# Kernel tuning notes

Hardware: AMD Instinct MI355X
Metric: run time of the kernel (lower is better)

The kernel has to match this reference:

```python
import jax, jax.numpy as jnp
import numpy as np

HEAD_DIM = 32
KS = 3        # kernel_size
DIL = 2       # dilation
SCALE = HEAD_DIM ** -0.5


def _unfold_1d(x, ks, dil):
    """Emulate nn.Unfold(ks, dil, dil*(ks-1)//2, 1) applied to x[:, :, :, None].

    x: [B, d, N]. The input is treated as an N x 1 image, so of the ks*ks
    window slots only the center width-column gathers real values; the rest
    are zero padding (faithful to the torch module).
    Returns [B, d, ks*ks, N].
    """
    B, d, N = x.shape
    pad = dil * (ks - 1) // 2
    xp = jnp.pad(x, ((0, 0), (0, 0), (pad, pad)))
    # shifted rows along the sequence (height) axis: [B, d, ks, N]
    rows = jnp.stack([xp[:, :, i * dil:i * dil + N] for i in range(ks)], axis=2)
    c = (ks - 1) // 2
    full = jnp.zeros((B, d, ks, ks, N), x.dtype).at[:, :, :, c, :].set(rows)
    return full.reshape(B, d, ks * ks, N)


def setup_inputs() -> dict:
    key = jax.random.key(0)
    kq, kk, kv = jax.random.split(key, 3)
    B, d, N = 4, 256, 8192
    return {
        "q": jax.random.normal(kq, (B, d, N), dtype=jnp.float32),
        "k": jax.random.normal(kk, (B, d, N), dtype=jnp.float32),
        "v": jax.random.normal(kv, (B, d, N), dtype=jnp.float32),
    }


def reference(q, k, v):
    B, d, N = q.shape
    h = d // HEAD_DIM
    K = KS * KS
    qh = q.reshape(B, h, HEAD_DIM, N)                       # [B,h,hd,N]
    kw = _unfold_1d(k, KS, DIL).reshape(B, h, HEAD_DIM, K, N)
    vw = _unfold_1d(v, KS, DIL).reshape(B, h, HEAD_DIM, K, N)
    attn = jnp.einsum('bhdn,bhdkn->bhnk', qh, kw) * SCALE    # [B,h,N,K]
    attn = jax.nn.softmax(attn, axis=-1)
    x = jnp.einsum('bhnk,bhdkn->bhnd', attn, vw)             # [B,h,N,hd]
    return x.transpose(0, 2, 1, 3).reshape(B, N, d)
```

## Files before the change

kernel.cpp:

```cpp
#include <hip/hip_runtime.h>


constexpr int Bn = 4;
constexpr int Dd = 256;
constexpr int Nn = 8192;
constexpr int HD = 32;
constexpr int Hh = Dd / HD;
constexpr float SCALE = 0.17677669529663687f;

typedef float vfloat4 __attribute__((ext_vector_type(4)));

__global__ __launch_bounds__(256) void dilate_attn_kernel(
    const float* __restrict__ q,
    const float* __restrict__ k,
    const float* __restrict__ v,
    float* __restrict__ out)
{
    const int tid     = threadIdx.x;
    const int lane    = tid & 63;
    const int sub     = lane & 15;
    const int quarter = lane >> 4;
    const int w       = tid >> 6;

    const int blk = blockIdx.x;
    const int bh  = blk >> 5;
    const int h   = bh & (Hh - 1);
    const int b   = bh >> 3;
    const int n0  = ((blk & 31) << 8) + (w << 6) + (sub << 2);

    const int cb = (b * Dd + h * HD + quarter * 8) * Nn + n0;
    const float* qb = q + cb;
    const float* kb = k + cb;
    const float* vb = v + cb;

    const bool hasL = (n0 >= 4);
    const bool hasR = (n0 + 4 < Nn);

    float s0[4] = {0.f, 0.f, 0.f, 0.f};
    float s1[4] = {0.f, 0.f, 0.f, 0.f};
    float s2[4] = {0.f, 0.f, 0.f, 0.f};
    #pragma unroll
    for (int c = 0; c < 8; ++c) {
        const int o = c * Nn;
        const float4 qc = *reinterpret_cast<const float4*>(qb + o);
        const float4 kc = *reinterpret_cast<const float4*>(kb + o);
        float2 km = make_float2(0.f, 0.f), kp = make_float2(0.f, 0.f);
        if (hasL) km = *reinterpret_cast<const float2*>(kb + o - 2);
        if (hasR) kp = *reinterpret_cast<const float2*>(kb + o + 4);
        s0[0] = fmaf(qc.x, km.x, s0[0]);
        s1[0] = fmaf(qc.x, kc.x, s1[0]);
        s2[0] = fmaf(qc.x, kc.z, s2[0]);
        s0[1] = fmaf(qc.y, km.y, s0[1]);
        s1[1] = fmaf(qc.y, kc.y, s1[1]);
        s2[1] = fmaf(qc.y, kc.w, s2[1]);
        s0[2] = fmaf(qc.z, kc.x, s0[2]);
        s1[2] = fmaf(qc.z, kc.z, s1[2]);
        s2[2] = fmaf(qc.z, kp.x, s2[2]);
        s0[3] = fmaf(qc.w, kc.y, s0[3]);
        s1[3] = fmaf(qc.w, kc.w, s1[3]);
        s2[3] = fmaf(qc.w, kp.y, s2[3]);
    }

    float p0[4], p1[4], p2[4];
    #pragma unroll
    for (int j = 0; j < 4; ++j) {
        float a = s0[j], bb = s1[j], cc = s2[j];
        a  += __shfl_xor(a, 16, 64);  a  += __shfl_xor(a, 32, 64);
        bb += __shfl_xor(bb, 16, 64); bb += __shfl_xor(bb, 32, 64);
        cc += __shfl_xor(cc, 16, 64); cc += __shfl_xor(cc, 32, 64);
        a *= SCALE; bb *= SCALE; cc *= SCALE;
        const float m  = fmaxf(fmaxf(a, bb), fmaxf(cc, 0.f));
        const float e0 = __expf(a - m);
        const float e1 = __expf(bb - m);
        const float e2 = __expf(cc - m);
        const float inv = 1.f / (e0 + e1 + e2 + 6.f * __expf(-m));
        p0[j] = e0 * inv; p1[j] = e1 * inv; p2[j] = e2 * inv;
    }

    float t[4][8];
    #pragma unroll
    for (int c = 0; c < 8; ++c) {
        const int o = c * Nn;
        const float4 vc = *reinterpret_cast<const float4*>(vb + o);
        float2 vm = make_float2(0.f, 0.f), vp = make_float2(0.f, 0.f);
        if (hasL) vm = *reinterpret_cast<const float2*>(vb + o - 2);
        if (hasR) vp = *reinterpret_cast<const float2*>(vb + o + 4);
        t[0][c] = fmaf(p0[0], vm.x, fmaf(p1[0], vc.x, p2[0] * vc.z));
        t[1][c] = fmaf(p0[1], vm.y, fmaf(p1[1], vc.y, p2[1] * vc.w));
        t[2][c] = fmaf(p0[2], vc.x, fmaf(p1[2], vc.z, p2[2] * vp.x));
        t[3][c] = fmaf(p0[3], vc.y, fmaf(p1[3], vc.w, p2[3] * vp.y));
    }

    float* ob = out + (b * Nn + n0) * Dd + h * HD + quarter * 8;
    #pragma unroll
    for (int j = 0; j < 4; ++j) {
        vfloat4* p = reinterpret_cast<vfloat4*>(ob + j * Dd);
        vfloat4 a = {t[j][0], t[j][1], t[j][2], t[j][3]};
        vfloat4 bq = {t[j][4], t[j][5], t[j][6], t[j][7]};
        __builtin_nontemporal_store(a, p);
        __builtin_nontemporal_store(bq, p + 1);
    }
}

extern "C" void kernel_launch(void* const* d_in, const int* in_sizes, int n_in,
                              void* d_out, int out_size, void* d_ws, size_t ws_size,
                              hipStream_t stream)
{
    const float* q = (const float*)d_in[0];
    const float* k = (const float*)d_in[1];
    const float* v = (const float*)d_in[2];
    float* out = (float*)d_out;

    const int total_threads = Bn * Hh * (Nn / 4) * 4;
    dilate_attn_kernel<<<total_threads / 256, 256, 0, stream>>>(q, k, v, out);
}
```

Before: 29.31 us.

## Stage K and V tiles with halos into LDS via direct global-to-LDS loads

K and V tiles of 32 rows by 128 columns, plus small halo columns, are copied into shared memory with global_load_lds. Neighbour taps then read from LDS instead of issuing overlapping misaligned float2 global loads. Q loads are hoisted ahead of the barrier so they overlap with the LDS fill. Blocks shrink to 128 threads, and the 36 KB of shared memory per block may limit occupancy.

```diff
diff --git a/kernel.cpp b/kernel.cpp
--- a/kernel.cpp
+++ b/kernel.cpp
@@ -1,4 +1,5 @@
 #include <hip/hip_runtime.h>
+#include <stdint.h>
 
 
 constexpr int Bn = 4;
@@ -6,34 +7,77 @@
 constexpr int Nn = 8192;
 constexpr int HD = 32;
 constexpr int Hh = Dd / HD;
+constexpr int NT = 128;
+constexpr int THREADS = 128;
 constexpr float SCALE = 0.17677669529663687f;
 
 typedef float vfloat4 __attribute__((ext_vector_type(4)));
 
-__global__ __launch_bounds__(256) void dilate_attn_kernel(
+__device__ __forceinline__ void gload_lds16(const float* g, float* l) {
+    __builtin_amdgcn_global_load_lds(
+        (const __attribute__((address_space(1))) void*)g,
+        (__attribute__((address_space(3))) void*)l, 16, 0, 0);
+}
+
+__global__ __launch_bounds__(THREADS) void dilate_attn_kernel(
     const float* __restrict__ q,
     const float* __restrict__ k,
     const float* __restrict__ v,
     float* __restrict__ out)
 {
+    __shared__ float kt[32 * NT];
+    __shared__ float vt[32 * NT];
+    __shared__ float khalo[32 * 8];
+    __shared__ float vhalo[32 * 8];
+
     const int tid     = threadIdx.x;
+    const int w       = tid >> 6;
     const int lane    = tid & 63;
-    const int sub     = lane & 15;
     const int quarter = lane >> 4;
-    const int w       = tid >> 6;
+    const int sub     = w * 16 + (lane & 15);
 
-    const int blk = blockIdx.x;
-    const int bh  = blk >> 5;
-    const int h   = bh & (Hh - 1);
-    const int b   = bh >> 3;
-    const int n0  = ((blk & 31) << 8) + (w << 6) + (sub << 2);
+    const int blk   = blockIdx.x;
+    const int bh    = blk >> 6;
+    const int blkn  = blk & 63;
+    const int h     = bh & (Hh - 1);
+    const int b     = bh >> 3;
+    const int nstart  = blkn * NT;
+    const int base_bh = (b * Dd + h * HD) * Nn;
 
-    const int cb = (b * Dd + h * HD + quarter * 8) * Nn + n0;
-    const float* qb = q + cb;
-    const float* kb = k + cb;
-    const float* vb = v + cb;
+    {
+        const int l31   = lane & 31;
+        const int rhalf = lane >> 5;
+        #pragma unroll
+        for (int i8 = 0; i8 < 8; ++i8) {
+            const int i   = w * 8 + i8;
+            const int row = 2 * i + rhalf;
+            gload_lds16(k + base_bh + row * Nn + nstart + l31 * 4, &kt[i * 256]);
+        }
+        #pragma unroll
+        for (int i8 = 0; i8 < 8; ++i8) {
+            const int i   = w * 8 + i8;
+            const int row = 2 * i + rhalf;
+            gload_lds16(v + base_bh + row * Nn + nstart + l31 * 4, &vt[i * 256]);
+        }
+        const int hch  = lane >> 1;
+        const int half = lane & 1;
+        int gcol = nstart + (half ? NT : -4);
+        gcol = gcol < 0 ? 0 : (gcol > Nn - 4 ? Nn - 4 : gcol);
+        if (w == 0) gload_lds16(k + base_bh + hch * Nn + gcol, &khalo[0]);
+        else        gload_lds16(v + base_bh + hch * Nn + gcol, &vhalo[0]);
+    }
 
-    const bool hasL = (n0 >= 4);
+    const int n0l = sub * 4;
+    const int n0  = nstart + n0l;
+    float4 qc[8];
+    const float* qb = q + base_bh + (quarter * 8) * Nn + nstart + n0l;
+    #pragma unroll
+    for (int c = 0; c < 8; ++c)
+        qc[c] = *reinterpret_cast<const float4*>(qb + c * Nn);
+
+    __syncthreads();
+
+    const bool hasL = (n0 >= 2);
     const bool hasR = (n0 + 4 < Nn);
 
     float s0[4] = {0.f, 0.f, 0.f, 0.f};
@@ -41,24 +85,26 @@
     float s2[4] = {0.f, 0.f, 0.f, 0.f};
     #pragma unroll
     for (int c = 0; c < 8; ++c) {
-        const int o = c * Nn;
-        const float4 qc = *reinterpret_cast<const float4*>(qb + o);
-        const float4 kc = *reinterpret_cast<const float4*>(kb + o);
-        float2 km = make_float2(0.f, 0.f), kp = make_float2(0.f, 0.f);
-        if (hasL) km = *reinterpret_cast<const float2*>(kb + o - 2);
-        if (hasR) kp = *reinterpret_cast<const float2*>(kb + o + 4);
-        s0[0] = fmaf(qc.x, km.x, s0[0]);
-        s1[0] = fmaf(qc.x, kc.x, s1[0]);
-        s2[0] = fmaf(qc.x, kc.z, s2[0]);
-        s0[1] = fmaf(qc.y, km.y, s0[1]);
-        s1[1] = fmaf(qc.y, kc.y, s1[1]);
-        s2[1] = fmaf(qc.y, kc.w, s2[1]);
-        s0[2] = fmaf(qc.z, kc.x, s0[2]);
-        s1[2] = fmaf(qc.z, kc.z, s1[2]);
-        s2[2] = fmaf(qc.z, kp.x, s2[2]);
-        s0[3] = fmaf(qc.w, kc.y, s0[3]);
-        s1[3] = fmaf(qc.w, kc.w, s1[3]);
-        s2[3] = fmaf(qc.w, kp.y, s2[3]);
+        const int row = quarter * 8 + c;
+        const float4 kc = *reinterpret_cast<const float4*>(&kt[row * NT + n0l]);
+        const float* pm = (sub == 0)  ? &khalo[row * 8 + 2] : &kt[row * NT + n0l - 2];
+        const float* pp = (sub == 31) ? &khalo[row * 8 + 4] : &kt[row * NT + n0l + 4];
+        const float2 kmr = *reinterpret_cast<const float2*>(pm);
+        const float2 kpr = *reinterpret_cast<const float2*>(pp);
+        const float2 km = hasL ? kmr : make_float2(0.f, 0.f);
+        const float2 kp = hasR ? kpr : make_float2(0.f, 0.f);
+        s0[0] = fmaf(qc[c].x, km.x, s0[0]);
+        s1[0] = fmaf(qc[c].x, kc.x, s1[0]);
+        s2[0] = fmaf(qc[c].x, kc.z, s2[0]);
+        s0[1] = fmaf(qc[c].y, km.y, s0[1]);
+        s1[1] = fmaf(qc[c].y, kc.y, s1[1]);
+        s2[1] = fmaf(qc[c].y, kc.w, s2[1]);
+        s0[2] = fmaf(qc[c].z, kc.x, s0[2]);
+        s1[2] = fmaf(qc[c].z, kc.z, s1[2]);
+        s2[2] = fmaf(qc[c].z, kp.x, s2[2]);
+        s0[3] = fmaf(qc[c].w, kc.y, s0[3]);
+        s1[3] = fmaf(qc[c].w, kc.w, s1[3]);
+        s2[3] = fmaf(qc[c].w, kp.y, s2[3]);
     }
 
     float p0[4], p1[4], p2[4];
@@ -80,11 +126,14 @@
     float t[4][8];
     #pragma unroll
     for (int c = 0; c < 8; ++c) {
-        const int o = c * Nn;
-        const float4 vc = *reinterpret_cast<const float4*>(vb + o);
-        float2 vm = make_float2(0.f, 0.f), vp = make_float2(0.f, 0.f);
-        if (hasL) vm = *reinterpret_cast<const float2*>(vb + o - 2);
-        if (hasR) vp = *reinterpret_cast<const float2*>(vb + o + 4);
+        const int row = quarter * 8 + c;
+        const float4 vc = *reinterpret_cast<const float4*>(&vt[row * NT + n0l]);
+        const float* pm = (sub == 0)  ? &vhalo[row * 8 + 2] : &vt[row * NT + n0l - 2];
+        const float* pp = (sub == 31) ? &vhalo[row * 8 + 4] : &vt[row * NT + n0l + 4];
+        const float2 vmr = *reinterpret_cast<const float2*>(pm);
+        const float2 vpr = *reinterpret_cast<const float2*>(pp);
+        const float2 vm = hasL ? vmr : make_float2(0.f, 0.f);
+        const float2 vp = hasR ? vpr : make_float2(0.f, 0.f);
         t[0][c] = fmaf(p0[0], vm.x, fmaf(p1[0], vc.x, p2[0] * vc.z));
         t[1][c] = fmaf(p0[1], vm.y, fmaf(p1[1], vc.y, p2[1] * vc.w));
         t[2][c] = fmaf(p0[2], vc.x, fmaf(p1[2], vc.z, p2[2] * vp.x));
@@ -95,10 +144,10 @@
     #pragma unroll
     for (int j = 0; j < 4; ++j) {
         vfloat4* p = reinterpret_cast<vfloat4*>(ob + j * Dd);
-        vfloat4 a = {t[j][0], t[j][1], t[j][2], t[j][3]};
-        vfloat4 bq = {t[j][4], t[j][5], t[j][6], t[j][7]};
-        __builtin_nontemporal_store(a, p);
-        __builtin_nontemporal_store(bq, p + 1);
+        vfloat4 a0 = {t[j][0], t[j][1], t[j][2], t[j][3]};
+        vfloat4 a1 = {t[j][4], t[j][5], t[j][6], t[j][7]};
+        __builtin_nontemporal_store(a0, p);
+        __builtin_nontemporal_store(a1, p + 1);
     }
 }
 
@@ -111,6 +160,6 @@
     const float* v = (const float*)d_in[2];
     float* out = (float*)d_out;
 
-    const int total_threads = Bn * Hh * (Nn / 4) * 4;
-    dilate_attn_kernel<<<total_threads / 256, 256, 0, stream>>>(q, k, v, out);
+    const int blocks = Bn * Hh * (Nn / NT);
+    dilate_attn_kernel<<<blocks, THREADS, 0, stream>>>(q, k, v, out);
 }
```

New measurement: 36.25 us. 23.7% more time.
